# Kernel optimization log

Measured on AMD Instinct MI355X. Metric: run time of the kernel, lower is better.

## Reference

```python
import jax, jax.numpy as jnp
import numpy as np

INPUT_DIM, HIDDEN_DIM, OUTPUT_DIM = 128, 256, 512
ALPHA = 0.1


def setup_inputs() -> dict:
    key = jax.random.key(0)
    ks = jax.random.split(key, 7)
    B, T = 64, 2048
    x = jax.random.normal(ks[0], (B, T, INPUT_DIM), dtype=jnp.float32)
    h0 = jax.random.normal(ks[1], (B, HIDDEN_DIM), dtype=jnp.float32)
    # torch nn.Linear weights: (out_features, in_features)
    s_xh = 1.0 / np.sqrt(INPUT_DIM)
    s_hh = 1.0 / np.sqrt(HIDDEN_DIM)
    W_xh_w = jax.random.uniform(ks[2], (HIDDEN_DIM, INPUT_DIM), jnp.float32, -s_xh, s_xh)
    W_xh_b = jax.random.uniform(ks[3], (HIDDEN_DIM,), jnp.float32, -s_xh, s_xh)
    W_hh_w = jax.random.uniform(ks[4], (HIDDEN_DIM, HIDDEN_DIM), jnp.float32, -s_hh, s_hh)
    W_hy_w = jax.random.uniform(ks[5], (OUTPUT_DIM, HIDDEN_DIM), jnp.float32, -s_hh, s_hh)
    W_hy_b = jax.random.uniform(ks[6], (OUTPUT_DIM,), jnp.float32, -s_hh, s_hh)
    return {"x": x, "h0": h0, "W_xh_w": W_xh_w, "W_xh_b": W_xh_b,
            "W_hh_w": W_hh_w, "W_hy_w": W_hy_w, "W_hy_b": W_hy_b}


def reference(x, h0, W_xh_w, W_xh_b, W_hh_w, W_hy_w, W_hy_b):
    # h[t] = (1-alpha)*h[t-1] + alpha*tanh(W_xh x[t] + b_xh + W_hh h[t-1])
    # y[t] = W_hy h[t] + b_hy
    # Precompute the input projection for all timesteps in one big GEMM.
    xp = jnp.einsum('bti,hi->bth', x, W_xh_w) + W_xh_b  # (B,T,H)

    def step(h, xp_t):
        pre = xp_t + jnp.einsum('bh,gh->bg', h, W_hh_w)
        h_new = (1.0 - ALPHA) * h + ALPHA * jnp.tanh(pre)
        return h_new, h_new

    _, h_all = jax.lax.scan(step, h0, jnp.swapaxes(xp, 0, 1))  # (T,B,H)
    h_all = jnp.swapaxes(h_all, 0, 1)  # (B,T,H)
    y = jnp.einsum('bth,oh->bto', h_all, W_hy_w) + W_hy_b  # (B,T,O)
    return y, h_all
```

## Files before the change

kernel.cpp:

```cpp
#include <hip/hip_runtime.h>
#include <hip/hip_bf16.h>

#define TT    2048
#define BATCH 64
#define IDIM  128
#define HDIM  256
#define ODIM  512
#define M1    (BATCH * TT)

typedef __bf16 bf16x4 __attribute__((ext_vector_type(4)));
typedef __bf16 bf16x8 __attribute__((ext_vector_type(8)));
typedef float  f32x4  __attribute__((ext_vector_type(4)));
typedef _Float16 f16;
typedef _Float16 f16x8 __attribute__((ext_vector_type(8)));

template<int BM, int NW, int N, int K>
__global__ __launch_bounds__(NW * 64)
void gemm_bt(const float* __restrict__ A, const float* __restrict__ Bw,
             const float* __restrict__ bias, float* __restrict__ C)
{
    constexpr int BN = NW * 64;
    constexpr int BK = 32;
    constexpr int PK = BK + 8;
    constexpr int MF = BM / 16;
    __shared__ __bf16 As[BM][PK];
    __shared__ __bf16 Bs[BN][PK];

    const int tid  = threadIdx.x;
    const int lane = tid & 63;
    const int wave = tid >> 6;
    const int l15  = lane & 15;
    const int l4   = lane >> 4;
    const long mrow = (long)blockIdx.x * BM;

    f32x4 acc[MF][4];
#pragma unroll
    for (int i = 0; i < MF; ++i)
#pragma unroll
        for (int j = 0; j < 4; ++j) acc[i][j] = (f32x4){0.f, 0.f, 0.f, 0.f};

    constexpr int THR   = NW * 64;
    constexpr int A_IT  = (BM * BK) / (THR * 4);
    constexpr int B_IT  = (BN * BK) / (THR * 4);

    for (int k0 = 0; k0 < K; k0 += BK) {
#pragma unroll
        for (int it = 0; it < A_IT; ++it) {
            int e = tid * 4 + it * THR * 4;
            int r = e / BK, c = e % BK;
            float4 v = *(const float4*)(A + (mrow + r) * K + (k0 + c));
            bf16x4 p = {(__bf16)v.x, (__bf16)v.y, (__bf16)v.z, (__bf16)v.w};
            *(bf16x4*)&As[r][c] = p;
        }
#pragma unroll
        for (int it = 0; it < B_IT; ++it) {
            int e = tid * 4 + it * THR * 4;
            int r = e / BK, c = e % BK;
            float4 v = *(const float4*)(Bw + (long)r * K + (k0 + c));
            bf16x4 p = {(__bf16)v.x, (__bf16)v.y, (__bf16)v.z, (__bf16)v.w};
            *(bf16x4*)&Bs[r][c] = p;
        }
        __syncthreads();

        const int kk = l4 * 8;
        bf16x8 a[MF], b[4];
#pragma unroll
        for (int mf = 0; mf < MF; ++mf)
            a[mf] = *(const bf16x8*)&As[mf * 16 + l15][kk];
#pragma unroll
        for (int nf = 0; nf < 4; ++nf)
            b[nf] = *(const bf16x8*)&Bs[wave * 64 + nf * 16 + l15][kk];
#pragma unroll
        for (int mf = 0; mf < MF; ++mf)
#pragma unroll
            for (int nf = 0; nf < 4; ++nf)
                acc[mf][nf] = __builtin_amdgcn_mfma_f32_16x16x32_bf16(
                    a[mf], b[nf], acc[mf][nf], 0, 0, 0);
        __syncthreads();
    }

#pragma unroll
    for (int nf = 0; nf < 4; ++nf) {
        const int col = wave * 64 + nf * 16 + l15;
        const float bv = bias[col];
#pragma unroll
        for (int mf = 0; mf < MF; ++mf) {
#pragma unroll
            for (int j = 0; j < 4; ++j) {
                long row = mrow + mf * 16 + l4 * 4 + j;
                C[row * N + col] = acc[mf][nf][j] + bv;
            }
        }
    }
}

__global__ __launch_bounds__(512, 1)
void rnn_scan_mfma(const float* __restrict__ xp, const float* __restrict__ h0,
                   const float* __restrict__ Whh, float* __restrict__ h_all)
{
    __shared__ f16 hs[2][HDIM];
    const int tid  = threadIdx.x;
    const int w    = tid >> 6;
    const int lane = tid & 63;
    const int q    = lane >> 4;
    const int c    = lane & 15;
    const int b    = blockIdx.x;

    const int mt  = c & 1;
    const int jj  = (c >> 1) & 3;
    const bool wr_en = (c >> 3) == 0;
    const int r   = 32 * w + 16 * mt + 4 * q + jj;

    f16x8 Wf[2][8];
#pragma unroll
    for (int m = 0; m < 2; ++m) {
        const float* wrp = Whh + (long)(32 * w + 16 * m + c) * HDIM + 8 * q;
#pragma unroll
        for (int kt = 0; kt < 8; ++kt) {
            f32x4 u0 = *(const f32x4*)(wrp + 32 * kt);
            f32x4 u1 = *(const f32x4*)(wrp + 32 * kt + 4);
            Wf[m][kt] = (f16x8){(f16)u0[0], (f16)u0[1], (f16)u0[2], (f16)u0[3],
                                (f16)u1[0], (f16)u1[1], (f16)u1[2], (f16)u1[3]};
        }
    }

    if (tid < HDIM) hs[0][tid] = (f16)h0[(long)b * HDIM + tid];
    float hold = h0[(long)b * HDIM + r];
    __syncthreads();

    const float* xpb = xp    + (long)b * TT * HDIM + r;
    float*       hab = h_all + (long)b * TT * HDIM + r;

    float xq0 = xpb[0];
    float xq1 = xpb[HDIM];

    for (int t = 0; t < TT; ++t) {
        const f16* hb = hs[t & 1];
        f16x8 Bf[8];
#pragma unroll
        for (int kt = 0; kt < 8; ++kt)
            Bf[kt] = *(const f16x8*)(hb + 32 * kt + 8 * q);

        const long tn = (long)((t + 2 < TT) ? (t + 2) : (TT - 1)) * HDIM;
        float xq2 = xpb[tn];

        f32x4 a0a = (f32x4){0.f,0.f,0.f,0.f}, a0b = (f32x4){0.f,0.f,0.f,0.f};
        f32x4 a1a = (f32x4){0.f,0.f,0.f,0.f}, a1b = (f32x4){0.f,0.f,0.f,0.f};
#pragma unroll
        for (int kt = 0; kt < 4; ++kt) {
            a0a = __builtin_amdgcn_mfma_f32_16x16x32_f16(Wf[0][kt],     Bf[kt],     a0a, 0, 0, 0);
            a1a = __builtin_amdgcn_mfma_f32_16x16x32_f16(Wf[1][kt],     Bf[kt],     a1a, 0, 0, 0);
            a0b = __builtin_amdgcn_mfma_f32_16x16x32_f16(Wf[0][kt + 4], Bf[kt + 4], a0b, 0, 0, 0);
            a1b = __builtin_amdgcn_mfma_f32_16x16x32_f16(Wf[1][kt + 4], Bf[kt + 4], a1b, 0, 0, 0);
        }
        f32x4 acc0 = a0a + a0b;
        f32x4 acc1 = a1a + a1b;

        float sx = (jj & 2) ? (mt ? acc1[2] : acc0[2]) : (mt ? acc1[0] : acc0[0]);
        float sy = (jj & 2) ? (mt ? acc1[3] : acc0[3]) : (mt ? acc1[1] : acc0[1]);
        float s  = (jj & 1) ? sy : sx;

        float pre = s + xq0;
        float e   = __expf(2.f * pre);
        float rc  = __builtin_amdgcn_rcpf(1.f + e);
        float hn  = fmaf(0.9f, hold, 0.1f) - 0.2f * rc;
        hold = hn;

        if (wr_en) {
            hs[(t + 1) & 1][r] = (f16)hn;
            hab[0] = hn;
        }
        hab += HDIM;
        xq0 = xq1; xq1 = xq2;

        __builtin_amdgcn_sched_barrier(0);
        asm volatile("s_waitcnt lgkmcnt(0)" ::: "memory");
        __builtin_amdgcn_s_barrier();
        __builtin_amdgcn_sched_barrier(0);
    }
}

extern "C" void kernel_launch(void* const* d_in, const int* in_sizes, int n_in,
                              void* d_out, int out_size, void* d_ws, size_t ws_size,
                              hipStream_t stream)
{
    const float* x   = (const float*)d_in[0];
    const float* h0  = (const float*)d_in[1];
    const float* Wxh = (const float*)d_in[2];
    const float* bxh = (const float*)d_in[3];
    const float* Whh = (const float*)d_in[4];
    const float* Why = (const float*)d_in[5];
    const float* bhy = (const float*)d_in[6];

    float* y     = (float*)d_out;
    float* h_all = y + (long)M1 * ODIM;
    float* xp    = y;

    gemm_bt<64, 4, HDIM, IDIM><<<M1 / 64, 4 * 64, 0, stream>>>(x, Wxh, bxh, xp);
    rnn_scan_mfma<<<BATCH, 512, 0, stream>>>(xp, h0, Whh, h_all);
    gemm_bt<64, 8, ODIM, HDIM><<<M1 / 64, 8 * 64, 0, stream>>>(h_all, Why, bhy, y);
}
```

Baseline: 1.181 ms.

## Halve scan block to 4 waves, each computing 64 hidden rows

The recurrent scan kernel now runs 256 threads (4 waves) per batch row instead of 512. Each wave holds W_hh fragments for 64 output rows and issues 8 MFMAs per k-half, so every lane produces a useful hidden value and the half-idle write lanes go away. The aim is to make the per-step barrier cheaper with fewer waves to synchronize. The cost is longer serial MFMA chains per wave and higher register pressure from holding twice as many weight fragments.

```diff
diff --git a/kernel.cpp b/kernel.cpp
--- a/kernel.cpp
+++ b/kernel.cpp
@@ -94,7 +94,7 @@
     }
 }
 
-__global__ __launch_bounds__(512, 1)
+__global__ __launch_bounds__(256, 1)
 void rnn_scan_mfma(const float* __restrict__ xp, const float* __restrict__ h0,
                    const float* __restrict__ Whh, float* __restrict__ h_all)
 {
@@ -106,25 +106,24 @@
     const int c    = lane & 15;
     const int b    = blockIdx.x;
 
-    const int mt  = c & 1;
-    const int jj  = (c >> 1) & 3;
-    const bool wr_en = (c >> 3) == 0;
-    const int r   = 32 * w + 16 * mt + 4 * q + jj;
-
-    f16x8 Wf[2][8];
-#pragma unroll
-    for (int m = 0; m < 2; ++m) {
-        const float* wrp = Whh + (long)(32 * w + 16 * m + c) * HDIM + 8 * q;
+    const int mtf = c & 3;
+    const int jj  = c >> 2;
+    const int r   = 64 * w + 16 * mtf + 4 * q + jj;
+
+    f16x8 Wf[4][8];
+#pragma unroll
+    for (int mt = 0; mt < 4; ++mt) {
+        const float* wrp = Whh + (long)(64 * w + 16 * mt + c) * HDIM + 8 * q;
 #pragma unroll
         for (int kt = 0; kt < 8; ++kt) {
             f32x4 u0 = *(const f32x4*)(wrp + 32 * kt);
             f32x4 u1 = *(const f32x4*)(wrp + 32 * kt + 4);
-            Wf[m][kt] = (f16x8){(f16)u0[0], (f16)u0[1], (f16)u0[2], (f16)u0[3],
-                                (f16)u1[0], (f16)u1[1], (f16)u1[2], (f16)u1[3]};
-        }
-    }
-
-    if (tid < HDIM) hs[0][tid] = (f16)h0[(long)b * HDIM + tid];
+            Wf[mt][kt] = (f16x8){(f16)u0[0], (f16)u0[1], (f16)u0[2], (f16)u0[3],
+                                 (f16)u1[0], (f16)u1[1], (f16)u1[2], (f16)u1[3]};
+        }
+    }
+
+    hs[0][tid] = (f16)h0[(long)b * HDIM + tid];
     float hold = h0[(long)b * HDIM + r];
     __syncthreads();
 
@@ -144,21 +143,29 @@
         const long tn = (long)((t + 2 < TT) ? (t + 2) : (TT - 1)) * HDIM;
         float xq2 = xpb[tn];
 
-        f32x4 a0a = (f32x4){0.f,0.f,0.f,0.f}, a0b = (f32x4){0.f,0.f,0.f,0.f};
-        f32x4 a1a = (f32x4){0.f,0.f,0.f,0.f}, a1b = (f32x4){0.f,0.f,0.f,0.f};
+        f32x4 aa[4], ab[4];
+#pragma unroll
+        for (int mt = 0; mt < 4; ++mt) {
+            aa[mt] = (f32x4){0.f, 0.f, 0.f, 0.f};
+            ab[mt] = (f32x4){0.f, 0.f, 0.f, 0.f};
+        }
 #pragma unroll
         for (int kt = 0; kt < 4; ++kt) {
-            a0a = __builtin_amdgcn_mfma_f32_16x16x32_f16(Wf[0][kt],     Bf[kt],     a0a, 0, 0, 0);
-            a1a = __builtin_amdgcn_mfma_f32_16x16x32_f16(Wf[1][kt],     Bf[kt],     a1a, 0, 0, 0);
-            a0b = __builtin_amdgcn_mfma_f32_16x16x32_f16(Wf[0][kt + 4], Bf[kt + 4], a0b, 0, 0, 0);
-            a1b = __builtin_amdgcn_mfma_f32_16x16x32_f16(Wf[1][kt + 4], Bf[kt + 4], a1b, 0, 0, 0);
-        }
-        f32x4 acc0 = a0a + a0b;
-        f32x4 acc1 = a1a + a1b;
-
-        float sx = (jj & 2) ? (mt ? acc1[2] : acc0[2]) : (mt ? acc1[0] : acc0[0]);
-        float sy = (jj & 2) ? (mt ? acc1[3] : acc0[3]) : (mt ? acc1[1] : acc0[1]);
-        float s  = (jj & 1) ? sy : sx;
+#pragma unroll
+            for (int mt = 0; mt < 4; ++mt) {
+                aa[mt] = __builtin_amdgcn_mfma_f32_16x16x32_f16(
+                    Wf[mt][kt],     Bf[kt],     aa[mt], 0, 0, 0);
+                ab[mt] = __builtin_amdgcn_mfma_f32_16x16x32_f16(
+                    Wf[mt][kt + 4], Bf[kt + 4], ab[mt], 0, 0, 0);
+            }
+        }
+
+        f32x4 s01 = (c & 1) ? (aa[1] + ab[1]) : (aa[0] + ab[0]);
+        f32x4 s23 = (c & 1) ? (aa[3] + ab[3]) : (aa[2] + ab[2]);
+        f32x4 sm  = (c & 2) ? s23 : s01;
+        float sx  = (jj & 2) ? sm[2] : sm[0];
+        float sy  = (jj & 2) ? sm[3] : sm[1];
+        float s   = (jj & 1) ? sy : sx;
 
         float pre = s + xq0;
         float e   = __expf(2.f * pre);
@@ -166,10 +173,8 @@
         float hn  = fmaf(0.9f, hold, 0.1f) - 0.2f * rc;
         hold = hn;
 
-        if (wr_en) {
-            hs[(t + 1) & 1][r] = (f16)hn;
-            hab[0] = hn;
-        }
+        hs[(t + 1) & 1][r] = (f16)hn;
+        hab[0] = hn;
         hab += HDIM;
         xq0 = xq1; xq1 = xq2;
 
@@ -197,6 +202,6 @@
     float* xp    = y;
 
     gemm_bt<64, 4, HDIM, IDIM><<<M1 / 64, 4 * 64, 0, stream>>>(x, Wxh, bxh, xp);
-    rnn_scan_mfma<<<BATCH, 512, 0, stream>>>(xp, h0, Whh, h_all);
+    rnn_scan_mfma<<<BATCH, 256, 0, stream>>>(xp, h0, Whh, h_all);
     gemm_bt<64, 8, ODIM, HDIM><<<M1 / 64, 8 * 64, 0, stream>>>(h_all, Why, bhy, y);
 }
```

Result: slower. 1.229 ms (+4.1%).
